# Kernel tuning notes

Hardware: AMD Instinct MI355X
Metric: run time of the kernel (lower is better)

Reference implementation:

```python
import jax, jax.numpy as jnp
import numpy as np

B, CIN, F, H, W = 4, 256, 128, 64, 64
EPS = 1e-5

def _conv1x1(x, Wm, b):
    # x: [B,C,H,W], Wm: [O,C] (1x1 conv kernel), b: [O]
    return jnp.einsum('bchw,oc->bohw', x, Wm) + b[None, :, None, None]

def setup_inputs() -> dict:
    key = jax.random.key(0)
    ks = jax.random.split(key, 11)
    s_in = 1.0 / np.sqrt(CIN)
    s_f = 1.0 / np.sqrt(F)
    return {
        'x':    jax.random.normal(ks[0], (B, CIN, H, W), jnp.float32),
        'Wg':   jax.random.normal(ks[1], (F, CIN), jnp.float32) * s_in,
        'bg':   jax.random.normal(ks[2], (F,), jnp.float32) * s_in,
        'Wt':   jax.random.normal(ks[3], (F, CIN), jnp.float32) * s_in,
        'bt':   jax.random.normal(ks[4], (F,), jnp.float32) * s_in,
        'Wp':   jax.random.normal(ks[5], (F, CIN), jnp.float32) * s_in,
        'bp':   jax.random.normal(ks[6], (F,), jnp.float32) * s_in,
        'Wz':   jax.random.normal(ks[7], (CIN, F), jnp.float32) * s_f,
        'bz':   jax.random.normal(ks[8], (CIN,), jnp.float32) * s_f,
        'ln_w': jax.random.normal(ks[9], (CIN, H, W), jnp.float32) * 0.1,
        'ln_b': jax.random.normal(ks[10], (CIN, H, W), jnp.float32) * 0.1,
    }

def reference(x, Wg, bg, Wt, bt, Wp, bp, Wz, bz, ln_w, ln_b):
    b, _, h, w = x.shape
    n = h * w
    # 1x1 conv projections
    g = _conv1x1(x, Wg, bg).reshape(b, F, n).transpose(0, 2, 1)      # [B,N,F]
    theta = _conv1x1(x, Wt, bt).reshape(b, F, n).transpose(0, 2, 1)  # [B,N,F]
    phi = _conv1x1(x, Wp, bp).reshape(b, F, n)                        # [B,F,N]
    # embedded-Gaussian affinity + softmax attention
    f = jnp.einsum('bnf,bfm->bnm', theta, phi)                        # [B,N,N]
    attn = jax.nn.softmax(f, axis=-1)
    y = jnp.einsum('bnm,bmf->bnf', attn, g)                           # [B,N,F]
    y = y.transpose(0, 2, 1).reshape(b, F, h, w)                      # [B,F,H,W]
    # output projection
    z = _conv1x1(y, Wz, bz)                                           # [B,CIN,H,W]
    # LayerNorm over (C,H,W) per sample, affine params shaped [C,H,W]
    mu = jnp.mean(z, axis=(1, 2, 3), keepdims=True)
    var = jnp.var(z, axis=(1, 2, 3), keepdims=True)
    z = (z - mu) * jax.lax.rsqrt(var + EPS)
    z = z * ln_w[None] + ln_b[None]
    return z + x
```

## Files before the change

### kernel.cpp

```cpp
#include <hip/hip_runtime.h>
#include <hip/hip_bf16.h>
#include <stdint.h>

#define CIN 256
#define FDIM 128
#define NSP 4096
#define EPS 1e-5f
#define LOG2E 1.4426950408889634f

typedef __attribute__((ext_vector_type(8))) short short8;
typedef __attribute__((ext_vector_type(4))) float f32x4;
typedef __attribute__((ext_vector_type(16))) float f32x16;

__device__ __forceinline__ short f2bf(float f) {
  union { float f; uint32_t u; } v; v.f = f;
  uint32_t r = v.u + 0x7fffu + ((v.u >> 16) & 1u);
  return (short)(r >> 16);
}
__device__ __forceinline__ float bf2f(short h) {
  union { uint32_t u; float f; } v; v.u = ((uint32_t)(uint16_t)h) << 16;
  return v.f;
}
__device__ __forceinline__ uint32_t pk2bf(float a, float b) {
  union { __hip_bfloat162 h; uint32_t u; } cv;
  cv.h = __float22bfloat162_rn(float2{a, b});
  return cv.u;
}
__device__ __forceinline__ void gload16(const void* g, void* l) {
  __builtin_amdgcn_global_load_lds(
      (const __attribute__((address_space(1))) unsigned int*)g,
      (__attribute__((address_space(3))) unsigned int*)l, 16, 0, 0);
}

__global__ void prep_weights(const float* __restrict__ Wg, const float* __restrict__ Wt,
                             const float* __restrict__ Wp, const float* __restrict__ Wz,
                             short* __restrict__ Wbf, short* __restrict__ Wzbf) {
  int idx = blockIdx.x * 256 + threadIdx.x;
  if (idx < 384 * 256) {
    int row = idx >> 8, col = idx & 255;
    float v;
    if (row < 128)       v = Wt[row * 256 + col] * LOG2E;
    else if (row < 256)  v = Wp[(row - 128) * 256 + col];
    else                 v = Wg[(row - 256) * 256 + col];
    Wbf[idx] = f2bf(v);
  } else {
    int j = idx - 384 * 256;
    if (j < 256 * 128) Wzbf[j] = f2bf(Wz[j]);
  }
}

__global__ void prep_xT(const float* __restrict__ x, short* __restrict__ xT) {
  __shared__ float tile[32][33];
  int b = blockIdx.z, c0 = blockIdx.y * 32, n0 = blockIdx.x * 32;
  int r = threadIdx.x >> 5, c = threadIdx.x & 31;
  const float* xb = x + (size_t)b * CIN * NSP;
#pragma unroll
  for (int k = 0; k < 4; k++)
    tile[r + 8 * k][c] = xb[(size_t)(c0 + r + 8 * k) * NSP + n0 + c];
  __syncthreads();
  short* xTb = xT + (size_t)b * NSP * CIN;
#pragma unroll
  for (int k = 0; k < 4; k++)
    xTb[(size_t)(n0 + r + 8 * k) * CIN + c0 + c] = f2bf(tile[c][r + 8 * k]);
}

__global__ void __launch_bounds__(256)
proj_kernel(const short* __restrict__ xT, const short* __restrict__ Wbf,
            const float* __restrict__ bt, const float* __restrict__ bp,
            const float* __restrict__ bg,
            short* __restrict__ theta, short* __restrict__ Kb, short* __restrict__ gT) {
  __shared__ short lds[5120];
  int bx = blockIdx.x;
  int b = bx >> 7;
  int n0 = (bx & 127) << 5;
  int p = blockIdx.y;
  int t = threadIdx.x, w = t >> 6, lane = t & 63, l15 = lane & 15, quad = lane >> 4;

  const short* arow = xT + (size_t)(b * NSP + n0 + (w & 1) * 16 + l15) * CIN;
  short8 a[8];
#pragma unroll
  for (int s = 0; s < 8; s++) a[s] = *(const short8*)(arow + s * 32 + quad * 8);

  const short* Wsrc = Wbf + p * 128 * 256;
  f32x4 zero = {0.f, 0.f, 0.f, 0.f};
  f32x4 acc[4];
#pragma unroll
  for (int i = 0; i < 4; i++) acc[i] = zero;

#pragma unroll
  for (int s = 0; s < 8; s++) {
#pragma unroll
    for (int ft = 0; ft < 4; ft++) {
      int ftg = (w >> 1) * 4 + ft;
      short8 bfr = *(const short8*)(Wsrc + (ftg * 16 + l15) * 256 + s * 32 + quad * 8);
      acc[ft] = __builtin_amdgcn_mfma_f32_16x16x32_bf16(a[s], bfr, acc[ft], 0, 0, 0);
    }
  }

  const float* bias = (p == 0) ? bt : (p == 1) ? bp : bg;
  if (p < 2) {
#pragma unroll
    for (int ft = 0; ft < 4; ft++) {
      int ftg = (w >> 1) * 4 + ft;
      float bv = bias[ftg * 16 + l15];
      if (p == 0) bv *= LOG2E;
#pragma unroll
      for (int rr = 0; rr < 4; rr++) {
        int n = (w & 1) * 16 + quad * 4 + rr;
        lds[n * 136 + ftg * 16 + l15] = f2bf(acc[ft][rr] + bv);
      }
    }
    __syncthreads();
    short* dst = ((p == 0) ? theta : Kb) + (size_t)(b * NSP + n0) * FDIM;
#pragma unroll
    for (int i = 0; i < 2; i++) {
      int flat = t + 256 * i;
      int row = flat >> 4, ch = flat & 15;
      *(short8*)(dst + (size_t)row * FDIM + ch * 8) = *(const short8*)(lds + row * 136 + ch * 8);
    }
  } else {
#pragma unroll
    for (int ft = 0; ft < 4; ft++) {
      int ftg = (w >> 1) * 4 + ft;
      float bv = bias[ftg * 16 + l15];
#pragma unroll
      for (int rr = 0; rr < 4; rr++) {
        int n = (w & 1) * 16 + quad * 4 + rr;
        lds[(ftg * 16 + l15) * 40 + n] = f2bf(acc[ft][rr] + bv);
      }
    }
    __syncthreads();
    short* dst = gT + (size_t)b * FDIM * NSP + n0;
#pragma unroll
    for (int i = 0; i < 2; i++) {
      int flat = t + 256 * i;
      int f = flat >> 2, c = flat & 3;
      *(short8*)(dst + (size_t)f * NSP + c * 8) = *(const short8*)(lds + f * 40 + c * 8);
    }
  }
}

__global__ void __launch_bounds__(256, 2)
flash_kernel(const short* __restrict__ thetab, const short* __restrict__ Kb,
             const short* __restrict__ gT, short* __restrict__ opart,
             float* __restrict__ lpart) {
  __shared__ __attribute__((aligned(16))) char smem[66048];
  short* Klds = (short*)smem;
  short* Vlds = (short*)(smem + 32768);
  float* Om   = (float*)smem;
  float* lsm  = (float*)(smem + 65536);

  const int bx = blockIdx.x;
  const int b  = bx >> 7;
  const int r  = bx & 127;
  const int q0 = (r >> 2) << 7;
  const int kc = r & 3;
  const int t = threadIdx.x, w = t >> 6, lane = t & 63;
  const int l31 = lane & 31, h = lane >> 5;
  const int qw = q0 + (w & 1) * 64;
  const int ck = w >> 1;

  const short* Qsrc = thetab + (size_t)b * NSP * FDIM;
  const short* Ksrc = Kb + (size_t)b * NSP * FDIM;
  const short* Vsrc = gT + (size_t)b * FDIM * NSP;

  short8 qf0[8], qf1[8];
#pragma unroll
  for (int s = 0; s < 8; s++) {
    qf0[s] = *(const short8*)(Qsrc + (size_t)(qw + l31) * FDIM + s * 16 + h * 8);
    qf1[s] = *(const short8*)(Qsrc + (size_t)(qw + 32 + l31) * FDIM + s * 16 + h * 8);
  }

  f32x16 O0[4], O1[4];
#pragma unroll
  for (int i = 0; i < 4; i++) {
#pragma unroll
    for (int j = 0; j < 16; j++) { O0[i][j] = 0.f; O1[i][j] = 0.f; }
  }
  float lsum0 = 0.f, lsum1 = 0.f;

  const int kA0 = kc << 10;

  auto stage = [&](int kA, int buf) {
#pragma unroll
    for (int e = 0; e < 4; e++) {
      int kr = (w << 2) + e;
      int row = (kr << 2) + (lane >> 4);
      int key = kA + (row & 31) + ((row >> 5) << 9);
      int gcol = (lane & 15) ^ (row & 15);
      gload16(Ksrc + (size_t)key * FDIM + gcol * 8,
              Klds + buf * 8192 + kr * 512);
    }
#pragma unroll
    for (int e = 0; e < 4; e++) {
      int vr = (w << 2) + e;
      int f = (vr << 3) + (lane >> 3);
      int m = (lane & 7) ^ (f & 7);
      int key = kA + ((m >> 2) << 9) + ((m & 3) << 3);
      gload16(Vsrc + (size_t)f * NSP + key,
              Vlds + buf * 8192 + vr * 512);
    }
  };

  stage(kA0, 0);
  __syncthreads();

  for (int it = 0; it < 16; ++it) {
    if (it + 1 < 16) stage(kA0 + (it + 1) * 32, (it + 1) & 1);
    const int cur = it & 1;
    const short* Kl = Klds + cur * 8192 + ck * 4096;
    const short* Vl = Vlds + cur * 8192;

    f32x16 S0, S1;
#pragma unroll
    for (int j = 0; j < 16; j++) { S0[j] = 0.f; S1[j] = 0.f; }
#pragma unroll
    for (int s = 0; s < 8; s++) {
      short8 ak = *(const short8*)(Kl + l31 * 128 + ((((s << 1) | h) ^ (l31 & 15)) << 3));
      S0 = __builtin_amdgcn_mfma_f32_32x32x16_bf16(ak, qf0[s], S0, 0, 0, 0);
      S1 = __builtin_amdgcn_mfma_f32_32x32x16_bf16(ak, qf1[s], S1, 0, 0, 0);
    }

    short8 Af0[2], Af1[2];
#pragma unroll
    for (int qb = 0; qb < 2; qb++) {
      float p[16];
      float ls = 0.f;
#pragma unroll
      for (int i = 0; i < 16; i++) {
        p[i] = exp2f(qb ? S1[i] : S0[i]);
        ls += p[i];
      }
      if (qb) lsum1 += ls; else lsum0 += ls;
      short8* Af = qb ? Af1 : Af0;
#pragma unroll
      for (int tt = 0; tt < 2; tt++) {
        const int rb = tt * 8;
        uint32_t pk01 = pk2bf(p[rb + 0], p[rb + 1]);
        uint32_t pk23 = pk2bf(p[rb + 2], p[rb + 3]);
        uint32_t pk45 = pk2bf(p[rb + 4], p[rb + 5]);
        uint32_t pk67 = pk2bf(p[rb + 6], p[rb + 7]);
        uint32_t r0 = (uint32_t)__shfl_xor((int)(h ? pk01 : pk45), 32, 64);
        uint32_t r1 = (uint32_t)__shfl_xor((int)(h ? pk23 : pk67), 32, 64);
        union { uint32_t u[4]; short8 v; } u;
        u.u[0] = h ? r0 : pk01;
        u.u[1] = h ? r1 : pk23;
        u.u[2] = h ? pk45 : r0;
        u.u[3] = h ? pk67 : r1;
        Af[tt] = u.v;
      }
    }

#pragma unroll
    for (int ft = 0; ft < 4; ft++) {
#pragma unroll
      for (int tt = 0; tt < 2; tt++) {
        short8 bv = *(const short8*)(Vl + ((ft * 32 + l31) << 6) +
                                     ((((ck << 2) | (tt << 1) | h) ^ (l31 & 7)) << 3));
        O0[ft] = __builtin_amdgcn_mfma_f32_32x32x16_bf16(Af0[tt], bv, O0[ft], 0, 0, 0);
        O1[ft] = __builtin_amdgcn_mfma_f32_32x32x16_bf16(Af1[tt], bv, O1[ft], 0, 0, 0);
      }
    }

    __syncthreads();
  }

  lsum0 += __shfl_xor(lsum0, 32, 64);
  lsum1 += __shfl_xor(lsum1, 32, 64);

  __syncthreads();
  if (w >= 2) {
    float* dst = Om + (size_t)(w - 2) * 8192;
#pragma unroll
    for (int qb = 0; qb < 2; qb++) {
#pragma unroll
      for (int ft = 0; ft < 4; ft++) {
#pragma unroll
        for (int reg = 0; reg < 16; reg++) {
          int rowq = qb * 32 + (reg & 3) + 8 * (reg >> 2) + 4 * h;
          dst[rowq * 128 + ft * 32 + l31] = qb ? O1[ft][reg] : O0[ft][reg];
        }
      }
    }
    if (h == 0) {
      lsm[(w - 2) * 64 + l31] = lsum0;
      lsm[(w - 2) * 64 + 32 + l31] = lsum1;
    }
  }
  __syncthreads();
  if (w < 2) {
    const float* src = Om + (size_t)w * 8192;
    short* od = opart + ((size_t)(kc * 4 + b) * NSP + qw) * FDIM;
#pragma unroll
    for (int qb = 0; qb < 2; qb++) {
#pragma unroll
      for (int ft = 0; ft < 4; ft++) {
#pragma unroll
        for (int reg = 0; reg < 16; reg++) {
          int rowq = qb * 32 + (reg & 3) + 8 * (reg >> 2) + 4 * h;
          float v = (qb ? O1[ft][reg] : O0[ft][reg]) + src[rowq * 128 + ft * 32 + l31];
          od[(size_t)rowq * FDIM + ft * 32 + l31] = f2bf(v);
        }
      }
    }
    if (h == 0) {
      size_t lb = (size_t)(kc * 4 + b) * NSP + qw;
      lpart[lb + l31] = lsum0 + lsm[w * 64 + l31];
      lpart[lb + 32 + l31] = lsum1 + lsm[w * 64 + 32 + l31];
    }
  }
}

__global__ void __launch_bounds__(256)
zproj_kernel(const short* __restrict__ opart, const float* __restrict__ lpart,
             const short* __restrict__ Wzbf, const float* __restrict__ bz,
             short* __restrict__ zb, float* __restrict__ psums) {
  __shared__ short ldsT[128 * 40];
  __shared__ float wsum[4][2];
  int bx = blockIdx.x;
  int b = bx >> 7;
  int n0 = (bx & 127) << 5;
  int ch0 = blockIdx.y * 128;
  int t = threadIdx.x, w = t >> 6, lane = t & 63, l15 = lane & 15, quad = lane >> 4;

  int row = n0 + (w & 1) * 16 + l15;
  float L = 0.f;
#pragma unroll
  for (int kcc = 0; kcc < 4; kcc++) L += lpart[(size_t)(kcc * 4 + b) * NSP + row];
  float inv = 1.0f / L;

  short8 a[4];
#pragma unroll
  for (int s = 0; s < 4; s++) {
    float accv[8] = {0, 0, 0, 0, 0, 0, 0, 0};
#pragma unroll
    for (int kcc = 0; kcc < 4; kcc++) {
      short8 v = *(const short8*)(opart + ((size_t)(kcc * 4 + b) * NSP + row) * FDIM + s * 32 + quad * 8);
#pragma unroll
      for (int j = 0; j < 8; j++) accv[j] += bf2f(v[j]);
    }
    short8 av;
#pragma unroll
    for (int j = 0; j < 8; j++) av[j] = f2bf(accv[j] * inv);
    a[s] = av;
  }

  f32x4 zero = {0.f, 0.f, 0.f, 0.f};
  f32x4 acc[4];
#pragma unroll
  for (int i = 0; i < 4; i++) acc[i] = zero;
#pragma unroll
  for (int s = 0; s < 4; s++) {
#pragma unroll
    for (int ct = 0; ct < 4; ct++) {
      int co = ch0 + (w >> 1) * 64 + ct * 16 + l15;
      short8 bfr = *(const short8*)(Wzbf + (size_t)co * FDIM + s * 32 + quad * 8);
      acc[ct] = __builtin_amdgcn_mfma_f32_16x16x32_bf16(a[s], bfr, acc[ct], 0, 0, 0);
    }
  }

  float s1 = 0.0f, s2 = 0.0f;
#pragma unroll
  for (int ct = 0; ct < 4; ct++) {
    int cg = (w >> 1) * 64 + ct * 16 + l15;
    float bv = bz[ch0 + cg];
#pragma unroll
    for (int rr = 0; rr < 4; rr++) {
      float v = acc[ct][rr] + bv;
      s1 += v; s2 += v * v;
      ldsT[cg * 40 + (w & 1) * 16 + quad * 4 + rr] = f2bf(v);
    }
  }
#pragma unroll
  for (int off = 32; off >= 1; off >>= 1) {
    s1 += __shfl_xor(s1, off, 64);
    s2 += __shfl_xor(s2, off, 64);
  }
  if (lane == 0) { wsum[w][0] = s1; wsum[w][1] = s2; }
  __syncthreads();
  if (t == 0) {
    int bid = blockIdx.y * 512 + bx;
    psums[bid * 2] = wsum[0][0] + wsum[1][0] + wsum[2][0] + wsum[3][0];
    psums[bid * 2 + 1] = wsum[0][1] + wsum[1][1] + wsum[2][1] + wsum[3][1];
  }
  short* dst = zb + (size_t)b * CIN * NSP + (size_t)ch0 * NSP + n0;
#pragma unroll
  for (int i = 0; i < 2; i++) {
    int flat = t + 256 * i;
    int c = flat >> 2, ch = flat & 3;
    *(short8*)(dst + (size_t)c * NSP + ch * 8) = *(const short8*)(ldsT + c * 40 + ch * 8);
  }
}

__global__ void reduce_sums(const float* __restrict__ psums, float* __restrict__ sums) {
  __shared__ float red[8];
  int t = threadIdx.x;
  if (t < 8) red[t] = 0.f;
  __syncthreads();
  for (int i = t; i < 1024; i += 256) {
    int b = (i & 511) >> 7;
    atomicAdd(&red[b * 2], psums[i * 2]);
    atomicAdd(&red[b * 2 + 1], psums[i * 2 + 1]);
  }
  __syncthreads();
  if (t < 8) sums[t] = red[t];
}

__global__ void __launch_bounds__(256)
finalize_kernel(const short* __restrict__ zbuf, const float* __restrict__ x,
                const float* __restrict__ lnw, const float* __restrict__ lnb,
                const float* __restrict__ sums, float* __restrict__ out) {
  int gid = blockIdx.x * 256 + threadIdx.x;
  size_t e0 = (size_t)gid * 8;
  int b = (int)(e0 >> 20);
  size_t ib = e0 & ((size_t)(1u << 20) - 1);
  float mean = sums[b * 2] * (1.0f / 1048576.0f);
  float var = sums[b * 2 + 1] * (1.0f / 1048576.0f) - mean * mean;
  float rs = rsqrtf(var + EPS);
  short8 zv = *(const short8*)(zbuf + e0);
#pragma unroll
  for (int k = 0; k < 8; k++) {
    float z = bf2f(zv[k]);
    out[e0 + k] = (z - mean) * rs * lnw[ib + k] + lnb[ib + k] + x[e0 + k];
  }
}

extern "C" void kernel_launch(void* const* d_in, const int* in_sizes, int n_in,
                              void* d_out, int out_size, void* d_ws, size_t ws_size,
                              hipStream_t stream) {
  const float* x   = (const float*)d_in[0];
  const float* Wg  = (const float*)d_in[1];
  const float* bg  = (const float*)d_in[2];
  const float* Wt  = (const float*)d_in[3];
  const float* bt  = (const float*)d_in[4];
  const float* Wp  = (const float*)d_in[5];
  const float* bp  = (const float*)d_in[6];
  const float* Wz  = (const float*)d_in[7];
  const float* bz  = (const float*)d_in[8];
  const float* lnw = (const float*)d_in[9];
  const float* lnb = (const float*)d_in[10];
  float* out = (float*)d_out;

  char* ws = (char*)d_ws;
  short* Wbf    = (short*)(ws);
  short* Wzbf   = (short*)(ws + 196608);
  short* xT     = (short*)(ws + 262144);
  short* opart  = (short*)(ws + 262144);
  float* lpart  = (float*)(ws + 17039360);
  short* thetab = (short*)(ws + 17301504);
  short* Kb     = (short*)(ws + 21495808);
  short* gT     = (short*)(ws + 25690112);
  short* zb     = (short*)(ws + 17301504);
  float* sums   = (float*)(ws + 29884416);
  float* psums  = (float*)(ws + 29884448);

  prep_weights<<<512, 256, 0, stream>>>(Wg, Wt, Wp, Wz, Wbf, Wzbf);
  prep_xT<<<dim3(128, 8, 4), 256, 0, stream>>>(x, xT);
  proj_kernel<<<dim3(512, 3), 256, 0, stream>>>(xT, Wbf, bt, bp, bg, thetab, Kb, gT);
  flash_kernel<<<512, 256, 0, stream>>>(thetab, Kb, gT, opart, lpart);
  zproj_kernel<<<dim3(512, 2), 256, 0, stream>>>(opart, lpart, Wzbf, bz, zb, psums);
  reduce_sums<<<1, 256, 0, stream>>>(psums, sums);
  finalize_kernel<<<2048, 256, 0, stream>>>(zb, x, lnw, lnb, sums, out);
}
```

Baseline: 211.7 us.

## Give each wave private K/V LDS tiles loaded via registers, drop block barriers

Replaces the block-shared double-buffered global_load_lds staging with per-wave private K and V tiles in padded LDS, loaded through registers. V for the next step is prefetched into registers before the PV MFMAs, and K is loaded after them. This removes the per-iteration __syncthreads, since each wave owns its own tile. In exchange the two waves that share a key range each load it separately, which duplicates global traffic. LDS use also grows, and the K load sits on the critical path with no prefetch.

```diff
diff --git a/kernel.cpp b/kernel.cpp
--- a/kernel.cpp
+++ b/kernel.cpp
@@ -25,11 +25,6 @@
   union { __hip_bfloat162 h; uint32_t u; } cv;
   cv.h = __float22bfloat162_rn(float2{a, b});
   return cv.u;
-}
-__device__ __forceinline__ void gload16(const void* g, void* l) {
-  __builtin_amdgcn_global_load_lds(
-      (const __attribute__((address_space(1))) unsigned int*)g,
-      (__attribute__((address_space(3))) unsigned int*)l, 16, 0, 0);
 }
 
 __global__ void prep_weights(const float* __restrict__ Wg, const float* __restrict__ Wt,
@@ -144,9 +139,9 @@
 flash_kernel(const short* __restrict__ thetab, const short* __restrict__ Kb,
              const short* __restrict__ gT, short* __restrict__ opart,
              float* __restrict__ lpart) {
-  __shared__ __attribute__((aligned(16))) char smem[66048];
+  __shared__ __attribute__((aligned(16))) char smem[75776];
   short* Klds = (short*)smem;
-  short* Vlds = (short*)(smem + 32768);
+  short* Vlds = (short*)(smem + 34816);
   float* Om   = (float*)smem;
   float* lsm  = (float*)(smem + 65536);
 
@@ -160,6 +155,9 @@
   const int qw = q0 + (w & 1) * 64;
   const int ck = w >> 1;
 
+  short* Kw = Klds + w * 4352;
+  short* Vw = Vlds + w * 5120;
+
   const short* Qsrc = thetab + (size_t)b * NSP * FDIM;
   const short* Ksrc = Kb + (size_t)b * NSP * FDIM;
   const short* Vsrc = gT + (size_t)b * FDIM * NSP;
@@ -179,44 +177,38 @@
   }
   float lsum0 = 0.f, lsum1 = 0.f;
 
-  const int kA0 = kc << 10;
-
-  auto stage = [&](int kA, int buf) {
-#pragma unroll
-    for (int e = 0; e < 4; e++) {
-      int kr = (w << 2) + e;
-      int row = (kr << 2) + (lane >> 4);
-      int key = kA + (row & 31) + ((row >> 5) << 9);
-      int gcol = (lane & 15) ^ (row & 15);
-      gload16(Ksrc + (size_t)key * FDIM + gcol * 8,
-              Klds + buf * 8192 + kr * 512);
-    }
-#pragma unroll
-    for (int e = 0; e < 4; e++) {
-      int vr = (w << 2) + e;
-      int f = (vr << 3) + (lane >> 3);
-      int m = (lane & 7) ^ (f & 7);
-      int key = kA + ((m >> 2) << 9) + ((m & 3) << 3);
-      gload16(Vsrc + (size_t)f * NSP + key,
-              Vlds + buf * 8192 + vr * 512);
-    }
-  };
-
-  stage(kA0, 0);
-  __syncthreads();
+  const int kbeg = (kc << 10) + ck * 512;
+  const int krow = lane >> 4, kcol = lane & 15;
+  const int vrow = lane >> 2, vcol = lane & 3;
+
+#pragma unroll
+  for (int e = 0; e < 8; e++) {
+    short8 kv = *(const short8*)(Ksrc + (size_t)(kbeg + e * 4 + krow) * FDIM + kcol * 8);
+    *(short8*)(Kw + (e * 4 + krow) * 136 + kcol * 8) = kv;
+  }
+#pragma unroll
+  for (int e = 0; e < 8; e++) {
+    short8 vv = *(const short8*)(Vsrc + (size_t)(e * 16 + vrow) * NSP + kbeg + vcol * 8);
+    *(short8*)(Vw + (e * 16 + vrow) * 40 + vcol * 8) = vv;
+  }
+
+  short8 nv[8];
 
   for (int it = 0; it < 16; ++it) {
-    if (it + 1 < 16) stage(kA0 + (it + 1) * 32, (it + 1) & 1);
-    const int cur = it & 1;
-    const short* Kl = Klds + cur * 8192 + ck * 4096;
-    const short* Vl = Vlds + cur * 8192;
+    const int kn = kbeg + (it + 1) * 32;
+
+    if (it > 0) {
+#pragma unroll
+      for (int e = 0; e < 8; e++)
+        *(short8*)(Vw + (e * 16 + vrow) * 40 + vcol * 8) = nv[e];
+    }
 
     f32x16 S0, S1;
 #pragma unroll
     for (int j = 0; j < 16; j++) { S0[j] = 0.f; S1[j] = 0.f; }
 #pragma unroll
     for (int s = 0; s < 8; s++) {
-      short8 ak = *(const short8*)(Kl + l31 * 128 + ((((s << 1) | h) ^ (l31 & 15)) << 3));
+      short8 ak = *(const short8*)(Kw + l31 * 136 + s * 16 + h * 8);
       S0 = __builtin_amdgcn_mfma_f32_32x32x16_bf16(ak, qf0[s], S0, 0, 0, 0);
       S1 = __builtin_amdgcn_mfma_f32_32x32x16_bf16(ak, qf1[s], S1, 0, 0, 0);
     }
@@ -251,18 +243,31 @@
       }
     }
 
+    if (it < 15) {
+#pragma unroll
+      for (int e = 0; e < 8; e++)
+        nv[e] = *(const short8*)(Vsrc + (size_t)(e * 16 + vrow) * NSP + kn + vcol * 8);
+    }
+
 #pragma unroll
     for (int ft = 0; ft < 4; ft++) {
 #pragma unroll
       for (int tt = 0; tt < 2; tt++) {
-        short8 bv = *(const short8*)(Vl + ((ft * 32 + l31) << 6) +
-                                     ((((ck << 2) | (tt << 1) | h) ^ (l31 & 7)) << 3));
+        short8 bv = *(const short8*)(Vw + (ft * 32 + l31) * 40 + tt * 16 + h * 8);
         O0[ft] = __builtin_amdgcn_mfma_f32_32x32x16_bf16(Af0[tt], bv, O0[ft], 0, 0, 0);
         O1[ft] = __builtin_amdgcn_mfma_f32_32x32x16_bf16(Af1[tt], bv, O1[ft], 0, 0, 0);
       }
     }
 
-    __syncthreads();
+    if (it < 15) {
+      short8 nk[8];
+#pragma unroll
+      for (int e = 0; e < 8; e++)
+        nk[e] = *(const short8*)(Ksrc + (size_t)(kn + e * 4 + krow) * FDIM + kcol * 8);
+#pragma unroll
+      for (int e = 0; e < 8; e++)
+        *(short8*)(Kw + (e * 4 + krow) * 136 + kcol * 8) = nk[e];
+    }
   }
 
   lsum0 += __shfl_xor(lsum0, 32, 64);
```

Result: slower. 222.7 us (+5.2%).
